# Kernel optimization log

Measured on AMD Instinct MI355X. Metric: run time of the kernel, lower is better.

## Reference

```python
import jax, jax.numpy as jnp
import numpy as np

BN_EPS = 1e-5


def setup_inputs() -> dict:
    key = jax.random.key(0)
    ks = jax.random.split(key, 8)
    B, S, D, H, O = 4, 25000, 128, 128, 128
    N, E = B * S, 600000
    x = jax.random.normal(ks[0], (B, S, D), dtype=jnp.float32)
    edge_index = jax.random.randint(ks[1], (2, E), 0, N)
    W1 = jax.random.normal(ks[2], (D, H), dtype=jnp.float32) * (1.0 / np.sqrt(D))
    b1 = jnp.zeros((H,), jnp.float32)
    gamma1 = jnp.ones((H,), jnp.float32)
    beta1 = jnp.zeros((H,), jnp.float32)
    W2 = jax.random.normal(ks[3], (H, O), dtype=jnp.float32) * (1.0 / np.sqrt(H))
    b2 = jnp.zeros((O,), jnp.float32)
    return {"x": x, "edge_index": edge_index, "W1": W1, "b1": b1,
            "gamma1": gamma1, "beta1": beta1, "W2": W2, "b2": b2}


def _gcn_norm(edge_index, num_nodes, dtype):
    # PyG gcn_norm: add self-loops, symmetric D^-1/2 (A+I) D^-1/2 edge weights.
    row, col = edge_index
    loop = jnp.arange(num_nodes, dtype=row.dtype)
    row_f = jnp.concatenate([row, loop])
    col_f = jnp.concatenate([col, loop])
    deg = jax.ops.segment_sum(jnp.ones(row_f.shape, dtype), row_f,
                              num_segments=num_nodes)
    dis = jnp.where(deg > 0, jax.lax.rsqrt(jnp.maximum(deg, 1e-12)), 0.0)
    norm = dis[row_f] * dis[col_f]  # [E + N]
    return row_f, col_f, norm


def _gcn_conv(h, W, b, row_f, col_f, norm, num_nodes):
    hw = h @ W                       # [N, out]
    msg = hw[col_f] * norm[:, None]  # gather + scale, [E+N, out]
    out = jax.ops.segment_sum(msg, row_f, num_segments=num_nodes)
    return out + b


def reference(x, edge_index, W1, b1, gamma1, beta1, W2, b2):
    B, S, D = x.shape
    N = B * S
    h = x.reshape(N, D)
    row_f, col_f, norm = _gcn_norm(edge_index, N, h.dtype)
    # layer 1: GCNConv -> BatchNorm (batch stats) -> ReLU (dropout inactive in eval)
    h = _gcn_conv(h, W1, b1, row_f, col_f, norm, N)
    mean = jnp.mean(h, axis=0)
    var = jnp.mean(jnp.square(h - mean), axis=0)
    h = gamma1 * (h - mean) * jax.lax.rsqrt(var + BN_EPS) + beta1
    h = jax.nn.relu(h)
    # layer 2: final GCNConv
    h = _gcn_conv(h, W2, b2, row_f, col_f, norm, N)
    return h.reshape(B, S, -1)
```

## Files before the change

kernel.cpp:

```cpp
#include <hip/hip_runtime.h>

#define DIM 128
#define BN_EPS 1e-5f

typedef short short8 __attribute__((ext_vector_type(8)));
typedef float floatx4 __attribute__((ext_vector_type(4)));

__device__ __forceinline__ unsigned short f2bf(float f) {
    unsigned int u = __builtin_bit_cast(unsigned int, f);
    u += 0x7FFFu + ((u >> 16) & 1u);
    return (unsigned short)(u >> 16);
}
__device__ __forceinline__ float bf2f(unsigned short h) {
    return __builtin_bit_cast(float, (unsigned int)h << 16);
}


__global__ void deg_kernel(const int* __restrict__ row, int* __restrict__ deg, int E) {
    int e = blockIdx.x * blockDim.x + threadIdx.x;
    if (e < E) atomicAdd(&deg[row[e]], 1);
}

__global__ void dis_kernel(const int* __restrict__ deg, float* __restrict__ dis, int n) {
    int i = blockIdx.x * blockDim.x + threadIdx.x;
    if (i < n) dis[i] = rsqrtf((float)(deg[i] + 1));
}


__global__ __launch_bounds__(256) void scan_block_kernel(const int* __restrict__ deg,
                                                         int* __restrict__ rowptr,
                                                         int* __restrict__ aux, int n) {
    __shared__ int ls[256];
    const int base = blockIdx.x * 1024;
    const int t = threadIdx.x;
    int v[4]; int s = 0;
    #pragma unroll
    for (int k = 0; k < 4; ++k) {
        int i = base + t * 4 + k;
        v[k] = (i < n) ? deg[i] : 0;
        s += v[k];
    }
    ls[t] = s;
    __syncthreads();
    for (int off = 1; off < 256; off <<= 1) {
        int x = (t >= off) ? ls[t - off] : 0;
        __syncthreads();
        ls[t] += x;
        __syncthreads();
    }
    int excl = ls[t] - s;
    if (t == 255) aux[blockIdx.x] = ls[255];
    #pragma unroll
    for (int k = 0; k < 4; ++k) {
        int i = base + t * 4 + k;
        if (i < n) rowptr[i] = excl;
        excl += v[k];
    }
}

__global__ void scan_aux_kernel(int* __restrict__ aux, int nb, int* __restrict__ rowptr, int n, int E) {
    int s = 0;
    for (int i = 0; i < nb; ++i) { int v = aux[i]; aux[i] = s; s += v; }
    rowptr[n] = E;
}

__global__ void add_offsets_kernel(int* __restrict__ rowptr, const int* __restrict__ aux, int n) {
    int i = blockIdx.x * blockDim.x + threadIdx.x;
    if (i < n) rowptr[i] += aux[i >> 10];
}


__global__ void scatter_kernel(const int* __restrict__ row, const int* __restrict__ col,
                               const float* __restrict__ dis, const int* __restrict__ rowptr,
                               int* __restrict__ cursor, int2* __restrict__ epack, int E) {
    int e = blockIdx.x * blockDim.x + threadIdx.x;
    if (e >= E) return;
    int r = row[e], c = col[e];
    int pos = rowptr[r] + atomicAdd(&cursor[r], 1);
    float nrm = dis[r] * dis[c];
    epack[pos] = make_int2(c, __builtin_bit_cast(int, nrm));
}


__global__ void convert_w_kernel(const float* __restrict__ W1, const float* __restrict__ W2,
                                 unsigned short* __restrict__ wfrag) {
    int s = blockIdx.x * blockDim.x + threadIdx.x;
    if (s >= 4096) return;
    int m  = s >> 11;
    int s2 = s & 2047;
    int kt = s2 >> 9;
    int nt = (s2 >> 6) & 7;
    int l  = s2 & 63;
    const float* W = m ? W2 : W1;
    unsigned short* o = wfrag + (size_t)m * 16384 + (size_t)s2 * 8;
    int k0 = kt * 32 + (l >> 4) * 8;
    int n0 = nt * 16 + (l & 15);
    #pragma unroll
    for (int j = 0; j < 8; ++j) o[j] = f2bf(W[(k0 + j) * DIM + n0]);
}


__global__ __launch_bounds__(256) void gemm_mfma_f32_kernel(
    const float* __restrict__ A, const unsigned short* __restrict__ wfrag,
    unsigned short* __restrict__ C, int n)
{
    __shared__ unsigned short sA[64][136];
    const int tid  = threadIdx.x;
    const int row0 = blockIdx.x * 64;

    #pragma unroll
    for (int l = 0; l < 8; ++l) {
        int idx = tid + l * 256;
        int r   = idx >> 5;
        int c4  = (idx & 31) * 4;
        float4 v;
        if (row0 + r < n) v = *(const float4*)(A + (size_t)(row0 + r) * DIM + c4);
        else              v = make_float4(0.f, 0.f, 0.f, 0.f);
        unsigned int lo = (unsigned int)f2bf(v.x) | ((unsigned int)f2bf(v.y) << 16);
        unsigned int hi = (unsigned int)f2bf(v.z) | ((unsigned int)f2bf(v.w) << 16);
        *(uint2*)(&sA[r][c4]) = make_uint2(lo, hi);
    }
    __syncthreads();

    const int wave = tid >> 6;
    const int lane = tid & 63;
    const int m    = lane & 15;
    const int quad = lane >> 4;
    const int rowA = wave * 16 + m;

    short8 af[4];
    #pragma unroll
    for (int kt = 0; kt < 4; ++kt)
        af[kt] = *(const short8*)(&sA[rowA][kt * 32 + quad * 8]);

    floatx4 acc[8];
    #pragma unroll
    for (int nt = 0; nt < 8; ++nt) acc[nt] = (floatx4){0.f, 0.f, 0.f, 0.f};

    #pragma unroll
    for (int nt = 0; nt < 8; ++nt)
        #pragma unroll
        for (int kt = 0; kt < 4; ++kt) {
            short8 bfr = *(const short8*)(wfrag + ((size_t)(kt * 8 + nt) * 64 + lane) * 8);
            acc[nt] = __builtin_amdgcn_mfma_f32_16x16x32_bf16(af[kt], bfr, acc[nt], 0, 0, 0);
        }

    #pragma unroll
    for (int nt = 0; nt < 8; ++nt)
        #pragma unroll
        for (int r = 0; r < 4; ++r) {
            int rr = row0 + wave * 16 + quad * 4 + r;
            if (rr < n) C[(size_t)rr * DIM + nt * 16 + m] = f2bf(acc[nt][r]);
        }
}


__global__ __launch_bounds__(256) void gemm_mfma_bn_kernel(
    const unsigned short* __restrict__ A, const unsigned short* __restrict__ wfrag,
    unsigned short* __restrict__ C, int n,
    const float* __restrict__ mean, const float* __restrict__ istd,
    const float* __restrict__ gamma, const float* __restrict__ beta)
{
    __shared__ unsigned short sA[64][136];
    const int tid  = threadIdx.x;
    const int row0 = blockIdx.x * 64;

    #pragma unroll
    for (int l = 0; l < 4; ++l) {
        int idx = tid + l * 256;
        int r   = idx >> 4;
        int c8  = (idx & 15) * 8;
        uint4 u = make_uint4(0, 0, 0, 0);
        if (row0 + r < n) u = *(const uint4*)(A + (size_t)(row0 + r) * DIM + c8);
        float f[8] = { bf2f((unsigned short)(u.x & 0xffff)), bf2f((unsigned short)(u.x >> 16)),
                       bf2f((unsigned short)(u.y & 0xffff)), bf2f((unsigned short)(u.y >> 16)),
                       bf2f((unsigned short)(u.z & 0xffff)), bf2f((unsigned short)(u.z >> 16)),
                       bf2f((unsigned short)(u.w & 0xffff)), bf2f((unsigned short)(u.w >> 16)) };
        #pragma unroll
        for (int k = 0; k < 8; ++k) {
            int c = c8 + k;
            f[k] = fmaxf(fmaf(gamma[c] * (f[k] - mean[c]), istd[c], beta[c]), 0.f);
        }
        uint4 o;
        o.x = (unsigned int)f2bf(f[0]) | ((unsigned int)f2bf(f[1]) << 16);
        o.y = (unsigned int)f2bf(f[2]) | ((unsigned int)f2bf(f[3]) << 16);
        o.z = (unsigned int)f2bf(f[4]) | ((unsigned int)f2bf(f[5]) << 16);
        o.w = (unsigned int)f2bf(f[6]) | ((unsigned int)f2bf(f[7]) << 16);
        *(uint4*)(&sA[r][c8]) = o;
    }
    __syncthreads();

    const int wave = tid >> 6;
    const int lane = tid & 63;
    const int m    = lane & 15;
    const int quad = lane >> 4;
    const int rowA = wave * 16 + m;

    short8 af[4];
    #pragma unroll
    for (int kt = 0; kt < 4; ++kt)
        af[kt] = *(const short8*)(&sA[rowA][kt * 32 + quad * 8]);

    floatx4 acc[8];
    #pragma unroll
    for (int nt = 0; nt < 8; ++nt) acc[nt] = (floatx4){0.f, 0.f, 0.f, 0.f};

    #pragma unroll
    for (int nt = 0; nt < 8; ++nt)
        #pragma unroll
        for (int kt = 0; kt < 4; ++kt) {
            short8 bfr = *(const short8*)(wfrag + ((size_t)(kt * 8 + nt) * 64 + lane) * 8);
            acc[nt] = __builtin_amdgcn_mfma_f32_16x16x32_bf16(af[kt], bfr, acc[nt], 0, 0, 0);
        }

    #pragma unroll
    for (int nt = 0; nt < 8; ++nt)
        #pragma unroll
        for (int r = 0; r < 4; ++r) {
            int rr = row0 + wave * 16 + quad * 4 + r;
            if (rr < n) C[(size_t)rr * DIM + nt * 16 + m] = f2bf(acc[nt][r]);
        }
}


template <bool OUT_BF16>
__global__ __launch_bounds__(256) void agg_csr_kernel(
    const unsigned short* __restrict__ hw, const float* __restrict__ dis,
    const int* __restrict__ rowptr, const int2* __restrict__ epack,
    const float* __restrict__ bias, void* __restrict__ out_, int n)
{
    const int sub  = threadIdx.x >> 4;
    const int l    = threadIdx.x & 15;
    const int node = blockIdx.x * 16 + sub;
    if (node >= n) return;
    const int j = l * 8;

    float acc[8];
    {
        const float d = dis[node];
        const float dd = d * d;
        uint4 u = *(const uint4*)(hw + (size_t)node * DIM + j);
        unsigned int uu[4] = {u.x, u.y, u.z, u.w};
        #pragma unroll
        for (int k = 0; k < 4; ++k) {
            acc[2*k]   = bf2f((unsigned short)(uu[k] & 0xffff)) * dd;
            acc[2*k+1] = bf2f((unsigned short)(uu[k] >> 16))    * dd;
        }
    }

    int p  = rowptr[node];
    const int pe = rowptr[node + 1];
    for (; p + 1 < pe; p += 2) {
        int2 e0 = epack[p], e1 = epack[p + 1];
        float w0 = __builtin_bit_cast(float, e0.y);
        float w1 = __builtin_bit_cast(float, e1.y);
        uint4 u0 = *(const uint4*)(hw + (size_t)e0.x * DIM + j);
        uint4 u1 = *(const uint4*)(hw + (size_t)e1.x * DIM + j);
        unsigned int a[4] = {u0.x, u0.y, u0.z, u0.w};
        unsigned int b[4] = {u1.x, u1.y, u1.z, u1.w};
        #pragma unroll
        for (int k = 0; k < 4; ++k) {
            acc[2*k]   = fmaf(bf2f((unsigned short)(a[k] & 0xffff)), w0, acc[2*k]);
            acc[2*k+1] = fmaf(bf2f((unsigned short)(a[k] >> 16)),    w0, acc[2*k+1]);
            acc[2*k]   = fmaf(bf2f((unsigned short)(b[k] & 0xffff)), w1, acc[2*k]);
            acc[2*k+1] = fmaf(bf2f((unsigned short)(b[k] >> 16)),    w1, acc[2*k+1]);
        }
    }
    if (p < pe) {
        int2 e = epack[p];
        float w = __builtin_bit_cast(float, e.y);
        uint4 u = *(const uint4*)(hw + (size_t)e.x * DIM + j);
        unsigned int a[4] = {u.x, u.y, u.z, u.w};
        #pragma unroll
        for (int k = 0; k < 4; ++k) {
            acc[2*k]   = fmaf(bf2f((unsigned short)(a[k] & 0xffff)), w, acc[2*k]);
            acc[2*k+1] = fmaf(bf2f((unsigned short)(a[k] >> 16)),    w, acc[2*k+1]);
        }
    }

    float4 b0 = *(const float4*)(bias + j);
    float4 b1 = *(const float4*)(bias + j + 4);
    acc[0] += b0.x; acc[1] += b0.y; acc[2] += b0.z; acc[3] += b0.w;
    acc[4] += b1.x; acc[5] += b1.y; acc[6] += b1.z; acc[7] += b1.w;

    if (OUT_BF16) {
        unsigned short* out = (unsigned short*)out_;
        uint4 o;
        o.x = (unsigned int)f2bf(acc[0]) | ((unsigned int)f2bf(acc[1]) << 16);
        o.y = (unsigned int)f2bf(acc[2]) | ((unsigned int)f2bf(acc[3]) << 16);
        o.z = (unsigned int)f2bf(acc[4]) | ((unsigned int)f2bf(acc[5]) << 16);
        o.w = (unsigned int)f2bf(acc[6]) | ((unsigned int)f2bf(acc[7]) << 16);
        *(uint4*)(out + (size_t)node * DIM + j) = o;
    } else {
        float* out = (float*)out_;
        *(float4*)(out + (size_t)node * DIM + j)     = make_float4(acc[0], acc[1], acc[2], acc[3]);
        *(float4*)(out + (size_t)node * DIM + j + 4) = make_float4(acc[4], acc[5], acc[6], acc[7]);
    }
}


__global__ __launch_bounds__(256) void stats_kernel(const unsigned short* __restrict__ h,
                                                    float* __restrict__ stat, int n)
{
    const int tid = threadIdx.x;
    const int cg  = tid & 15;
    const int rg  = tid >> 4;
    float s[8], q[8];
    #pragma unroll
    for (int k = 0; k < 8; ++k) { s[k] = 0.f; q[k] = 0.f; }

    const int stride = gridDim.x * 16;
    for (int i = blockIdx.x * 16 + rg; i < n; i += 2 * stride) {
        uint4 u0 = *(const uint4*)(h + (size_t)i * DIM + cg * 8);
        int i1 = i + stride;
        uint4 u1 = (i1 < n) ? *(const uint4*)(h + (size_t)i1 * DIM + cg * 8)
                            : make_uint4(0, 0, 0, 0);
        unsigned int a[4] = {u0.x, u0.y, u0.z, u0.w};
        unsigned int b[4] = {u1.x, u1.y, u1.z, u1.w};
        #pragma unroll
        for (int k = 0; k < 4; ++k) {
            float a0 = bf2f((unsigned short)(a[k] & 0xffff));
            float a1 = bf2f((unsigned short)(a[k] >> 16));
            float c0 = bf2f((unsigned short)(b[k] & 0xffff));
            float c1 = bf2f((unsigned short)(b[k] >> 16));
            s[2*k]   += a0 + c0;
            s[2*k+1] += a1 + c1;
            q[2*k]   = fmaf(a0, a0, fmaf(c0, c0, q[2*k]));
            q[2*k+1] = fmaf(a1, a1, fmaf(c1, c1, q[2*k+1]));
        }
    }

    __shared__ float red[16][128];
    #pragma unroll
    for (int k = 0; k < 8; ++k) red[rg][cg * 8 + k] = s[k];
    __syncthreads();
    if (tid < 128) {
        float t = 0.f;
        #pragma unroll
        for (int r = 0; r < 16; ++r) t += red[r][tid];
        atomicAdd(&stat[tid], t);
    }
    __syncthreads();
    #pragma unroll
    for (int k = 0; k < 8; ++k) red[rg][cg * 8 + k] = q[k];
    __syncthreads();
    if (tid < 128) {
        float t = 0.f;
        #pragma unroll
        for (int r = 0; r < 16; ++r) t += red[r][tid];
        atomicAdd(&stat[DIM + tid], t);
    }
}

__global__ void bn_finalize_kernel(const float* __restrict__ stat, float* __restrict__ mi, int n) {
    int j = threadIdx.x;
    if (j < DIM) {
        float mean = stat[j] / (float)n;
        float var  = stat[DIM + j] / (float)n - mean * mean;
        mi[j]       = mean;
        mi[DIM + j] = rsqrtf(var + BN_EPS);
    }
}


extern "C" void kernel_launch(void* const* d_in, const int* in_sizes, int n_in,
                              void* d_out, int out_size, void* d_ws, size_t ws_size,
                              hipStream_t stream)
{
    const float* x      = (const float*)d_in[0];
    const int*   ei     = (const int*)  d_in[1];
    const float* W1     = (const float*)d_in[2];
    const float* b1     = (const float*)d_in[3];
    const float* gamma1 = (const float*)d_in[4];
    const float* beta1  = (const float*)d_in[5];
    const float* W2     = (const float*)d_in[6];
    const float* b2     = (const float*)d_in[7];
    float* out = (float*)d_out;

    const int N = in_sizes[0] / DIM;
    const int E = in_sizes[1] / 2;
    const int* row = ei;
    const int* col = ei + E;

    const int NB = (N + 1023) / 1024;

    unsigned short* hw    = (unsigned short*)d_ws;
    unsigned short* h1    = hw + (size_t)N * DIM;
    int2*  epack  = (int2*)(h1 + (size_t)N * DIM);
    unsigned short* wfrag = (unsigned short*)(epack + E);
    float* dis    = (float*)(wfrag + 2 * 16384);
    int*   deg    = (int*)(dis + N);
    int*   cursor = deg + N;
    int*   rowptr = cursor + N;
    int*   aux    = rowptr + N + 1;
    float* stat   = (float*)(aux + 128);
    float* mi     = stat + 256;

    hipMemsetAsync(deg,    0, (size_t)N * sizeof(int), stream);
    hipMemsetAsync(cursor, 0, (size_t)N * sizeof(int), stream);
    hipMemsetAsync(stat,   0, 256 * sizeof(float), stream);

    deg_kernel<<<(E + 255) / 256, 256, 0, stream>>>(row, deg, E);
    dis_kernel<<<(N + 255) / 256, 256, 0, stream>>>(deg, dis, N);
    scan_block_kernel<<<NB, 256, 0, stream>>>(deg, rowptr, aux, N);
    scan_aux_kernel<<<1, 1, 0, stream>>>(aux, NB, rowptr, N, E);
    add_offsets_kernel<<<(N + 255) / 256, 256, 0, stream>>>(rowptr, aux, N);
    scatter_kernel<<<(E + 255) / 256, 256, 0, stream>>>(row, col, dis, rowptr, cursor,
                                                        epack, E);
    convert_w_kernel<<<16, 256, 0, stream>>>(W1, W2, wfrag);

    gemm_mfma_f32_kernel<<<(N + 63) / 64, 256, 0, stream>>>(x, wfrag, hw, N);
    agg_csr_kernel<true><<<(N + 15) / 16, 256, 0, stream>>>(hw, dis, rowptr, epack, b1, h1, N);
    stats_kernel<<<512, 256, 0, stream>>>(h1, stat, N);
    bn_finalize_kernel<<<1, DIM, 0, stream>>>(stat, mi, N);

    gemm_mfma_bn_kernel<<<(N + 63) / 64, 256, 0, stream>>>(h1, wfrag + 16384, hw, N,
                                                           mi, mi + DIM, gamma1, beta1);
    agg_csr_kernel<false><<<(N + 15) / 16, 256, 0, stream>>>(hw, dis, rowptr, epack, b2, out, N);
}
```

Baseline: 315.8 us.

## Sort nodes by degree for balanced aggregation and unroll edge loop by four

Builds a per-degree histogram in the scan kernel and a degree-bucketed node permutation, so that each aggregation block processes nodes of similar degree and wavefront divergence from mixed edge counts is reduced. It also folds the dis computation into the scan kernel, dropping one launch, and adds a 4-way unrolled edge loop to keep more gathers in flight. In exchange it adds atomics and a serial histogram prefix in a single thread, plus an indirection through perm that scatters node writes and loses locality in output stores.

```diff
diff --git a/kernel.cpp b/kernel.cpp
--- a/kernel.cpp
+++ b/kernel.cpp
@@ -2,6 +2,7 @@
 
 #define DIM 128
 #define BN_EPS 1e-5f
+#define NBUCK 512
 
 typedef short short8 __attribute__((ext_vector_type(8)));
 typedef float floatx4 __attribute__((ext_vector_type(4)));
@@ -21,18 +22,17 @@
     if (e < E) atomicAdd(&deg[row[e]], 1);
 }
 
-__global__ void dis_kernel(const int* __restrict__ deg, float* __restrict__ dis, int n) {
-    int i = blockIdx.x * blockDim.x + threadIdx.x;
-    if (i < n) dis[i] = rsqrtf((float)(deg[i] + 1));
-}
-
 
 __global__ __launch_bounds__(256) void scan_block_kernel(const int* __restrict__ deg,
                                                          int* __restrict__ rowptr,
-                                                         int* __restrict__ aux, int n) {
+                                                         int* __restrict__ aux,
+                                                         float* __restrict__ dis,
+                                                         int* __restrict__ hist, int n) {
     __shared__ int ls[256];
+    __shared__ int lh[NBUCK];
     const int base = blockIdx.x * 1024;
     const int t = threadIdx.x;
+    lh[t] = 0; lh[t + 256] = 0;
     int v[4]; int s = 0;
     #pragma unroll
     for (int k = 0; k < 4; ++k) {
@@ -42,6 +42,14 @@
     }
     ls[t] = s;
     __syncthreads();
+    #pragma unroll
+    for (int k = 0; k < 4; ++k) {
+        int i = base + t * 4 + k;
+        if (i < n) {
+            dis[i] = rsqrtf((float)(v[k] + 1));
+            atomicAdd(&lh[min(v[k], NBUCK - 1)], 1);
+        }
+    }
     for (int off = 1; off < 256; off <<= 1) {
         int x = (t >= off) ? ls[t - off] : 0;
         __syncthreads();
@@ -56,17 +64,30 @@
         if (i < n) rowptr[i] = excl;
         excl += v[k];
     }
-}
-
-__global__ void scan_aux_kernel(int* __restrict__ aux, int nb, int* __restrict__ rowptr, int n, int E) {
+    __syncthreads();
+    if (lh[t])       atomicAdd(&hist[t],       lh[t]);
+    if (lh[t + 256]) atomicAdd(&hist[t + 256], lh[t + 256]);
+}
+
+__global__ void scan_aux_kernel(int* __restrict__ aux, int nb, int* __restrict__ rowptr,
+                                int n, int E, const int* __restrict__ hist,
+                                int* __restrict__ histbase) {
     int s = 0;
     for (int i = 0; i < nb; ++i) { int v = aux[i]; aux[i] = s; s += v; }
     rowptr[n] = E;
-}
-
-__global__ void add_offsets_kernel(int* __restrict__ rowptr, const int* __restrict__ aux, int n) {
+    s = 0;
+    for (int i = 0; i < NBUCK; ++i) { int v = hist[i]; histbase[i] = s; s += v; }
+}
+
+__global__ void finalize_nodes_kernel(int* __restrict__ rowptr, const int* __restrict__ aux,
+                                      const int* __restrict__ deg, int* __restrict__ histbase,
+                                      int* __restrict__ perm, int n) {
     int i = blockIdx.x * blockDim.x + threadIdx.x;
-    if (i < n) rowptr[i] += aux[i >> 10];
+    if (i >= n) return;
+    rowptr[i] += aux[i >> 10];
+    int b = min(deg[i], NBUCK - 1);
+    int pos = atomicAdd(&histbase[b], 1);
+    perm[pos] = i;
 }
 
 
@@ -227,12 +248,14 @@
 __global__ __launch_bounds__(256) void agg_csr_kernel(
     const unsigned short* __restrict__ hw, const float* __restrict__ dis,
     const int* __restrict__ rowptr, const int2* __restrict__ epack,
+    const int* __restrict__ perm,
     const float* __restrict__ bias, void* __restrict__ out_, int n)
 {
     const int sub  = threadIdx.x >> 4;
     const int l    = threadIdx.x & 15;
-    const int node = blockIdx.x * 16 + sub;
-    if (node >= n) return;
+    const int slot = blockIdx.x * 16 + sub;
+    if (slot >= n) return;
+    const int node = perm[slot];
     const int j = l * 8;
 
     float acc[8];
@@ -250,6 +273,34 @@
 
     int p  = rowptr[node];
     const int pe = rowptr[node + 1];
+
+    for (; p + 3 < pe; p += 4) {
+        int2 e0 = epack[p],     e1 = epack[p + 1];
+        int2 e2 = epack[p + 2], e3 = epack[p + 3];
+        float w0 = __builtin_bit_cast(float, e0.y);
+        float w1 = __builtin_bit_cast(float, e1.y);
+        float w2 = __builtin_bit_cast(float, e2.y);
+        float w3 = __builtin_bit_cast(float, e3.y);
+        uint4 u0 = *(const uint4*)(hw + (size_t)e0.x * DIM + j);
+        uint4 u1 = *(const uint4*)(hw + (size_t)e1.x * DIM + j);
+        uint4 u2 = *(const uint4*)(hw + (size_t)e2.x * DIM + j);
+        uint4 u3 = *(const uint4*)(hw + (size_t)e3.x * DIM + j);
+        unsigned int a[4] = {u0.x, u0.y, u0.z, u0.w};
+        unsigned int b[4] = {u1.x, u1.y, u1.z, u1.w};
+        unsigned int c[4] = {u2.x, u2.y, u2.z, u2.w};
+        unsigned int d[4] = {u3.x, u3.y, u3.z, u3.w};
+        #pragma unroll
+        for (int k = 0; k < 4; ++k) {
+            acc[2*k]   = fmaf(bf2f((unsigned short)(a[k] & 0xffff)), w0, acc[2*k]);
+            acc[2*k+1] = fmaf(bf2f((unsigned short)(a[k] >> 16)),    w0, acc[2*k+1]);
+            acc[2*k]   = fmaf(bf2f((unsigned short)(b[k] & 0xffff)), w1, acc[2*k]);
+            acc[2*k+1] = fmaf(bf2f((unsigned short)(b[k] >> 16)),    w1, acc[2*k+1]);
+            acc[2*k]   = fmaf(bf2f((unsigned short)(c[k] & 0xffff)), w2, acc[2*k]);
+            acc[2*k+1] = fmaf(bf2f((unsigned short)(c[k] >> 16)),    w2, acc[2*k+1]);
+            acc[2*k]   = fmaf(bf2f((unsigned short)(d[k] & 0xffff)), w3, acc[2*k]);
+            acc[2*k+1] = fmaf(bf2f((unsigned short)(d[k] >> 16)),    w3, acc[2*k+1]);
+        }
+    }
     for (; p + 1 < pe; p += 2) {
         int2 e0 = epack[p], e1 = epack[p + 1];
         float w0 = __builtin_bit_cast(float, e0.y);
@@ -395,26 +446,32 @@
     int*   aux    = rowptr + N + 1;
     float* stat   = (float*)(aux + 128);
     float* mi     = stat + 256;
+    int*   perm   = (int*)(mi + 256);
+    int*   hist   = perm + N;
+    int*   histbase = hist + NBUCK;
 
     hipMemsetAsync(deg,    0, (size_t)N * sizeof(int), stream);
     hipMemsetAsync(cursor, 0, (size_t)N * sizeof(int), stream);
     hipMemsetAsync(stat,   0, 256 * sizeof(float), stream);
+    hipMemsetAsync(hist,   0, NBUCK * sizeof(int), stream);
 
     deg_kernel<<<(E + 255) / 256, 256, 0, stream>>>(row, deg, E);
-    dis_kernel<<<(N + 255) / 256, 256, 0, stream>>>(deg, dis, N);
-    scan_block_kernel<<<NB, 256, 0, stream>>>(deg, rowptr, aux, N);
-    scan_aux_kernel<<<1, 1, 0, stream>>>(aux, NB, rowptr, N, E);
-    add_offsets_kernel<<<(N + 255) / 256, 256, 0, stream>>>(rowptr, aux, N);
+    scan_block_kernel<<<NB, 256, 0, stream>>>(deg, rowptr, aux, dis, hist, N);
+    scan_aux_kernel<<<1, 1, 0, stream>>>(aux, NB, rowptr, N, E, hist, histbase);
+    finalize_nodes_kernel<<<(N + 255) / 256, 256, 0, stream>>>(rowptr, aux, deg, histbase,
+                                                               perm, N);
     scatter_kernel<<<(E + 255) / 256, 256, 0, stream>>>(row, col, dis, rowptr, cursor,
                                                         epack, E);
     convert_w_kernel<<<16, 256, 0, stream>>>(W1, W2, wfrag);
 
     gemm_mfma_f32_kernel<<<(N + 63) / 64, 256, 0, stream>>>(x, wfrag, hw, N);
-    agg_csr_kernel<true><<<(N + 15) / 16, 256, 0, stream>>>(hw, dis, rowptr, epack, b1, h1, N);
+    agg_csr_kernel<true><<<(N + 15) / 16, 256, 0, stream>>>(hw, dis, rowptr, epack, perm,
+                                                            b1, h1, N);
     stats_kernel<<<512, 256, 0, stream>>>(h1, stat, N);
     bn_finalize_kernel<<<1, DIM, 0, stream>>>(stat, mi, N);
 
     gemm_mfma_bn_kernel<<<(N + 63) / 64, 256, 0, stream>>>(h1, wfrag + 16384, hw, N,
                                                            mi, mi + DIM, gamma1, beta1);
-    agg_csr_kernel<false><<<(N + 15) / 16, 256, 0, stream>>>(hw, dis, rowptr, epack, b2, out, N);
-}
+    agg_csr_kernel<false><<<(N + 15) / 16, 256, 0, stream>>>(hw, dis, rowptr, epack, perm,
+                                                             b2, out, N);
+}
```

New measurement: 702.3 us. +122.4%, slower.
